# Kernel tuning notes

Measured on AMD Instinct MI355X. Metric: run time of the kernel, lower is better.

The kernel has to match this reference:

```python
import jax, jax.numpy as jnp
import numpy as np

B, T, NC, WD, UNITS = 128, 256, 128, 512, 512
IN_DIM = NC + WD + NC  # x_char + x_word + one-hot prev word


def setup_inputs() -> dict:
    key = jax.random.key(0)
    ks = jax.random.split(key, 7)
    scale = 0.05  # keep gates out of saturation
    return {
        "x_char": jax.random.normal(ks[0], (B, T, NC), jnp.float32),
        "x_word": jax.random.normal(ks[1], (B, T, WD), jnp.float32),
        "W": jax.random.normal(ks[2], (IN_DIM, 4 * UNITS), jnp.float32) * scale,
        "U": jax.random.normal(ks[3], (UNITS, 4 * UNITS), jnp.float32) * scale,
        "b": jnp.zeros((4 * UNITS,), jnp.float32),
        "Ws": jax.random.normal(ks[4], (UNITS, NC), jnp.float32) * scale,
        "bs": jnp.zeros((NC,), jnp.float32),
    }


def reference(x_char, x_word, W, U, b, Ws, bs):
    Bsz, Tlen, nclasses = x_char.shape
    units = U.shape[0]
    # time-major, concat char+word features (matches x_shuffled in original)
    x_t = jnp.concatenate(
        [jnp.swapaxes(x_char, 0, 1), jnp.swapaxes(x_word, 0, 1)], axis=-1
    )  # [T, B, NC+WD]
    word0 = jnp.full((Bsz, nclasses), 1e-5, x_char.dtype)  # start_char
    h0 = jnp.zeros((Bsz, units), x_char.dtype)
    c0 = jnp.zeros((Bsz, units), x_char.dtype)

    def step(carry, x_i):
        word_vec, h, c = carry
        ins = jnp.concatenate([x_i, word_vec], axis=1)  # [B, IN_DIM]
        z = ins @ W + h @ U + b  # [B, 4*units]; Keras gate order i,f,c,o
        zi, zf, zg, zo = jnp.split(z, 4, axis=1)
        i = jax.nn.sigmoid(zi)
        f = jax.nn.sigmoid(zf)
        g = jnp.tanh(zg)
        o = jax.nn.sigmoid(zo)
        c_new = f * c + i * g
        h_new = o * jnp.tanh(c_new)
        probs = jax.nn.softmax(h_new @ Ws + bs, axis=-1)
        idx = jnp.argmax(probs, axis=1)  # [B]
        word_vec_new = jax.nn.one_hot(idx, nclasses, dtype=x_char.dtype)
        return (word_vec_new, h_new, c_new), idx

    _, idxs = jax.lax.scan(step, (word0, h0, c0), x_t)  # idxs: [T, B]
    return jnp.swapaxes(idxs, 0, 1)  # [B, T] int word indices
```

## Files before the change

### kernel.cpp

```cpp
#include <hip/hip_runtime.h>
#include <math.h>

#define BSZ   128
#define TLEN  256
#define NCLS  128
#define WDIM  512
#define XDIM  640
#define G4    2048

#define BT    16
#define JTS   16
#define NBLK  256
#define NTHR  512
#define KCH   8

#define H_OFF     0
#define LPART_OFF 131072
#define W0_OFF    1179648
#define FLAG_OFF  1181696

typedef unsigned long long ull;

__device__ __forceinline__ float sigmoidf_(float x) {
  return 1.0f / (1.0f + expf(-x));
}

__device__ __forceinline__ float4 ld_dev16(const float* p) {
  const ull* q = (const ull*)p;
  ull a = __hip_atomic_load(q,     __ATOMIC_RELAXED, __HIP_MEMORY_SCOPE_AGENT);
  ull b = __hip_atomic_load(q + 1, __ATOMIC_RELAXED, __HIP_MEMORY_SCOPE_AGENT);
  float4 r;
  ((ull*)&r)[0] = a;
  ((ull*)&r)[1] = b;
  return r;
}

__device__ __forceinline__ void st_dev16(float* p, float4 v) {
  ull* q = (ull*)p;
  __hip_atomic_store(q,     ((ull*)&v)[0], __ATOMIC_RELAXED, __HIP_MEMORY_SCOPE_AGENT);
  __hip_atomic_store(q + 1, ((ull*)&v)[1], __ATOMIC_RELAXED, __HIP_MEMORY_SCOPE_AGENT);
}

__global__ void setup_kernel(const float* __restrict__ W,
                             const float* __restrict__ bias,
                             float* __restrict__ ws) {
  int tid = blockIdx.x * blockDim.x + threadIdx.x;
  if (tid < 4096)
    ((unsigned int*)(ws + FLAG_OFF))[tid] = 0u;
  if (tid < G4) {
    float s = 0.0f;
    #pragma unroll 4
    for (int r = 0; r < NCLS; ++r)
      s += W[(size_t)(XDIM + r) * G4 + tid];
    ws[W0_OFF + tid] = bias[tid] + 1e-5f * s;
  }
}

__global__ void __launch_bounds__(NTHR, 1)
lstm_main(const float* __restrict__ xc, const float* __restrict__ xw,
          const float* __restrict__ W,  const float* __restrict__ U,
          const float* __restrict__ bias, const float* __restrict__ Wsm,
          const float* __restrict__ bsv, int* __restrict__ out,
          float* __restrict__ ws)
{
  __shared__ float U_lds[512 * 64];
  __shared__ float ins_lds[2][2176];
  __shared__ float wsm_lds[16 * 128];
  __shared__ float hl_lds[16 * 17];
  __shared__ int   idx_lds[BT];

  float* zred  = &ins_lds[0][0];
  float* Wt    = &ins_lds[0][0];
  float* red_v = zred;
  int*   red_i = (int*)(zred + 528);

  const int tid = threadIdx.x;
  const int blk = blockIdx.x;
  const int grp = blk & 7;
  const int jt  = blk >> 3;
  const int b0  = grp * BT;
  const int j0  = jt * JTS;

  const int gb  = tid & 15;
  const int gg  = (tid >> 4) & 3;
  const int j4  = (tid >> 6) & 3;
  const int kh  = tid >> 8;
  const int c0  = gg * 512 + j0 + j4 * 4;
  const int cc0 = gg * 16 + j4 * 4;

  const int srow = tid >> 5;
  const int sseg = tid & 31;

  const int ub = tid >> 5;
  const int um = tid & 31;

  const int vb = (tid >> 4) & 15;
  const int vj = tid & 15;

  float* hbuf   = ws + H_OFF;
  float* lpart  = ws + LPART_OFF;
  unsigned int* flags = (unsigned int*)(ws + FLAG_OFF);
  unsigned int* myflag   = flags + (grp * 32 + jt) * 16;
  unsigned int* pollflag = flags + (grp * 32 + (tid & 31)) * 16;

  {
    int cc  = tid & 63;
    int col = (cc >> 4) * 512 + j0 + (cc & 15);
    int k0  = tid >> 6;
    for (int kk = 0; kk < 64; ++kk) {
      int k = kk * 8 + k0;
      U_lds[k * 64 + cc] = U[(size_t)k * G4 + col];
    }
  }
  {
    int row = tid >> 5, col4 = tid & 31;
    *(float4*)(&wsm_lds[row * 128 + col4 * 4]) =
        *(const float4*)(Wsm + (size_t)(j0 + row) * NCLS + col4 * 4);
  }

  float4 xq[KCH];
  auto chunk_gemm = [&](int tt0) {
    #pragma unroll
    for (int s = 0; s < KCH; ++s) xq[s] = make_float4(0.f, 0.f, 0.f, 0.f);
    #pragma unroll 1
    for (int kt = 0; kt < 10; ++kt) {
      int id0 = tid,       k0t = id0 >> 4, cg0 = id0 & 15;
      int id1 = tid + 512, k1t = id1 >> 4, cg1 = id1 & 15;
      int col0 = (cg0 >> 2) * 512 + j0 + (cg0 & 3) * 4;
      int col1 = (cg1 >> 2) * 512 + j0 + (cg1 & 3) * 4;
      float4 wv0 = *(const float4*)(W + (size_t)(kt * 64 + k0t) * G4 + col0);
      float4 wv1 = *(const float4*)(W + (size_t)(kt * 64 + k1t) * G4 + col1);
      __syncthreads();
      *(float4*)(Wt + k0t * 64 + cg0 * 4) = wv0;
      *(float4*)(Wt + k1t * 64 + cg1 * 4) = wv1;
      __syncthreads();
      const float* wp = Wt + (kh * 32) * 64 + cc0;
      const float* xb0 = (kt < 2)
        ? xc + ((size_t)(b0 + gb) * TLEN + tt0) * NCLS + kt * 64 + kh * 32
        : xw + ((size_t)(b0 + gb) * TLEN + tt0) * WDIM + (kt * 64 - 128) + kh * 32;
      const size_t xstr = (kt < 2) ? (size_t)NCLS : (size_t)WDIM;
      #pragma unroll
      for (int sb = 0; sb < 2; ++sb) {
        #pragma unroll 1
        for (int q = 0; q < 8; ++q) {
          const float* wq = wp + q * 4 * 64;
          float4 w0 = *(const float4*)(wq);
          float4 w1 = *(const float4*)(wq + 64);
          float4 w2 = *(const float4*)(wq + 128);
          float4 w3 = *(const float4*)(wq + 192);
          const float* xquad = xb0 + (size_t)(sb * 4) * xstr + q * 4;
          #pragma unroll
          for (int u = 0; u < 4; ++u) {
            const int s = sb * 4 + u;
            float4 xa = *(const float4*)(xquad + (size_t)u * xstr);
            xq[s].x = fmaf(xa.x, w0.x, xq[s].x);
            xq[s].y = fmaf(xa.x, w0.y, xq[s].y);
            xq[s].z = fmaf(xa.x, w0.z, xq[s].z);
            xq[s].w = fmaf(xa.x, w0.w, xq[s].w);
            xq[s].x = fmaf(xa.y, w1.x, xq[s].x);
            xq[s].y = fmaf(xa.y, w1.y, xq[s].y);
            xq[s].z = fmaf(xa.y, w1.z, xq[s].z);
            xq[s].w = fmaf(xa.y, w1.w, xq[s].w);
            xq[s].x = fmaf(xa.z, w2.x, xq[s].x);
            xq[s].y = fmaf(xa.z, w2.y, xq[s].y);
            xq[s].z = fmaf(xa.z, w2.z, xq[s].z);
            xq[s].w = fmaf(xa.z, w2.w, xq[s].w);
            xq[s].x = fmaf(xa.w, w3.x, xq[s].x);
            xq[s].y = fmaf(xa.w, w3.y, xq[s].y);
            xq[s].z = fmaf(xa.w, w3.z, xq[s].z);
            xq[s].w = fmaf(xa.w, w3.w, xq[s].w);
          }
          __builtin_amdgcn_sched_barrier(0);
        }
      }
    }
  };

  float creg = 0.0f;

  __syncthreads();
  chunk_gemm(0);
  __syncthreads();

  for (int t = 0; t < TLEN; ++t) {
    float4 acc = xq[0];
    #pragma unroll
    for (int s = 0; s < KCH - 1; ++s) xq[s] = xq[s + 1];

    if (t == 0) {
      if (kh == 0) {
        const float4 w0 = *(const float4*)(ws + W0_OFF + c0);
        acc.x += w0.x; acc.y += w0.y; acc.z += w0.z; acc.w += w0.w;
      }
    } else {
      {
        const float* pb = lpart
            + (((size_t)((t - 1) & 1) * NBLK) + grp * 32) * (BT * NCLS)
            + (size_t)ub * NCLS + um * 4;
        float4 s0 = make_float4(0.f, 0.f, 0.f, 0.f);
        float4 s1 = s0, s2 = s0, s3 = s0;
        #pragma unroll 1
        for (int j2 = 0; j2 < 32; j2 += 4) {
          float4 a = ld_dev16(pb + (size_t)(j2 + 0) * (BT * NCLS));
          float4 b = ld_dev16(pb + (size_t)(j2 + 1) * (BT * NCLS));
          float4 c = ld_dev16(pb + (size_t)(j2 + 2) * (BT * NCLS));
          float4 d = ld_dev16(pb + (size_t)(j2 + 3) * (BT * NCLS));
          s0.x += a.x; s0.y += a.y; s0.z += a.z; s0.w += a.w;
          s1.x += b.x; s1.y += b.y; s1.z += b.z; s1.w += b.w;
          s2.x += c.x; s2.y += c.y; s2.z += c.z; s2.w += c.w;
          s3.x += d.x; s3.y += d.y; s3.z += d.z; s3.w += d.w;
        }
        float4 lv;
        lv.x = (s0.x + s1.x) + (s2.x + s3.x);
        lv.y = (s0.y + s1.y) + (s2.y + s3.y);
        lv.z = (s0.z + s1.z) + (s2.z + s3.z);
        lv.w = (s0.w + s1.w) + (s2.w + s3.w);
        const float4 bb = *(const float4*)(bsv + um * 4);
        float bv = lv.x + bb.x; int bi = um * 4;
        if (lv.y + bb.y > bv) { bv = lv.y + bb.y; bi = um * 4 + 1; }
        if (lv.z + bb.z > bv) { bv = lv.z + bb.z; bi = um * 4 + 2; }
        if (lv.w + bb.w > bv) { bv = lv.w + bb.w; bi = um * 4 + 3; }
        red_v[ub * 33 + um] = bv; red_i[ub * 33 + um] = bi;
        __syncthreads();
        if (um == 0) {
          float v = red_v[ub * 33]; int vi = red_i[ub * 33];
          #pragma unroll
          for (int s = 1; s < 32; ++s) {
            float v2 = red_v[ub * 33 + s];
            int   i2 = red_i[ub * 33 + s];
            if (v2 > v || (v2 == v && i2 < vi)) { v = v2; vi = i2; }
          }
          idx_lds[ub] = vi;
          if (jt == 0) out[(b0 + ub) * TLEN + (t - 1)] = vi;
        }
        __syncthreads();
      }
      if (kh == 0) {
        int wr = XDIM + idx_lds[gb];
        const float4 b4 = *(const float4*)(bias + c0);
        const float4 w4 = *(const float4*)(W + (size_t)wr * G4 + c0);
        acc.x += b4.x + w4.x;  acc.y += b4.y + w4.y;
        acc.z += b4.z + w4.z;  acc.w += b4.w + w4.w;
      }
      {
        const float* hprev = hbuf + ((t + 1) & 1) * (BSZ * 512);
        {
          float4 r = ld_dev16(hprev + (size_t)(b0 + srow) * 512 + sseg * 4);
          *(float4*)(&ins_lds[0][srow * 132 + sseg * 4]) = r;
          __syncthreads();
        }
        #pragma unroll 1
        for (int ch = 0; ch < 4; ++ch) {
          float4 nxt;
          if (ch + 1 < 4) {
            nxt = ld_dev16(hprev + (size_t)(b0 + srow) * 512
                           + (ch + 1) * 128 + sseg * 4);
          }
          const float* up = U_lds + (ch * 128 + kh * 64) * 64 + cc0;
          const float* ip = &ins_lds[ch & 1][gb * 132 + kh * 64];
          #pragma unroll 8
          for (int kk = 0; kk < 64; ++kk) {
            float a = ip[kk];
            float4 u4 = *(const float4*)(up + kk * 64);
            acc.x = fmaf(a, u4.x, acc.x);
            acc.y = fmaf(a, u4.y, acc.y);
            acc.z = fmaf(a, u4.z, acc.z);
            acc.w = fmaf(a, u4.w, acc.w);
          }
          if (ch + 1 < 4) {
            *(float4*)(&ins_lds[(ch + 1) & 1][srow * 132 + sseg * 4]) = nxt;
            __syncthreads();
          }
        }
      }
    }

    *(float4*)(zred + (gb * 2 + kh) * 68 + cc0) = acc;
    __syncthreads();

    if (tid < 256) {
      float zi = zred[(vb * 2) * 68 +  0 + vj] + zred[(vb * 2 + 1) * 68 +  0 + vj];
      float zf = zred[(vb * 2) * 68 + 16 + vj] + zred[(vb * 2 + 1) * 68 + 16 + vj];
      float zg = zred[(vb * 2) * 68 + 32 + vj] + zred[(vb * 2 + 1) * 68 + 32 + vj];
      float zo = zred[(vb * 2) * 68 + 48 + vj] + zred[(vb * 2 + 1) * 68 + 48 + vj];
      float iv = sigmoidf_(zi);
      float fv = sigmoidf_(zf);
      float gv = tanhf(zg);
      float ov = sigmoidf_(zo);
      creg = fv * creg + iv * gv;
      float hn = ov * tanhf(creg);
      __hip_atomic_store(hbuf + (t & 1) * (BSZ * 512)
                         + (size_t)(b0 + vb) * 512 + j0 + vj, hn,
                         __ATOMIC_RELAXED, __HIP_MEMORY_SCOPE_AGENT);
      hl_lds[vb * 17 + vj] = hn;
    }
    __syncthreads();

    {
      float p0 = 0.f, p1 = 0.f, p2 = 0.f, p3 = 0.f;
      #pragma unroll
      for (int j = 0; j < 16; ++j) {
        float hv = hl_lds[ub * 17 + j];
        const float4 wv = *(const float4*)(&wsm_lds[j * 128 + um * 4]);
        p0 = fmaf(hv, wv.x, p0); p1 = fmaf(hv, wv.y, p1);
        p2 = fmaf(hv, wv.z, p2); p3 = fmaf(hv, wv.w, p3);
      }
      float* dst = lpart
          + (((size_t)(t & 1) * NBLK) + (grp * 32 + jt)) * (BT * NCLS)
          + (size_t)ub * NCLS + um * 4;
      st_dev16(dst, make_float4(p0, p1, p2, p3));
    }

    __syncthreads();
    if (tid == 0)
      __hip_atomic_store(myflag, (unsigned)(t + 1),
                         __ATOMIC_RELAXED, __HIP_MEMORY_SCOPE_AGENT);
    if (((t + 1) & (KCH - 1)) == 0 && t + 1 < TLEN)
      chunk_gemm(t + 1);
    if (tid < 64) {
      const unsigned tgt = (unsigned)(t + 1);
      for (;;) {
        unsigned v = __hip_atomic_load(pollflag, __ATOMIC_RELAXED,
                                       __HIP_MEMORY_SCOPE_AGENT);
        if (__all(v >= tgt)) break;
        __builtin_amdgcn_s_sleep(1);
      }
    }
    __syncthreads();
  }

  if (jt == 0) {
    const float* pb = lpart
        + (((size_t)((TLEN - 1) & 1) * NBLK) + grp * 32) * (BT * NCLS)
        + (size_t)ub * NCLS + um * 4;
    float4 s0 = make_float4(0.f, 0.f, 0.f, 0.f);
    float4 s1 = s0, s2 = s0, s3 = s0;
    #pragma unroll 1
    for (int j2 = 0; j2 < 32; j2 += 4) {
      float4 a = ld_dev16(pb + (size_t)(j2 + 0) * (BT * NCLS));
      float4 b = ld_dev16(pb + (size_t)(j2 + 1) * (BT * NCLS));
      float4 c = ld_dev16(pb + (size_t)(j2 + 2) * (BT * NCLS));
      float4 d = ld_dev16(pb + (size_t)(j2 + 3) * (BT * NCLS));
      s0.x += a.x; s0.y += a.y; s0.z += a.z; s0.w += a.w;
      s1.x += b.x; s1.y += b.y; s1.z += b.z; s1.w += b.w;
      s2.x += c.x; s2.y += c.y; s2.z += c.z; s2.w += c.w;
      s3.x += d.x; s3.y += d.y; s3.z += d.z; s3.w += d.w;
    }
    float4 lv;
    lv.x = (s0.x + s1.x) + (s2.x + s3.x);
    lv.y = (s0.y + s1.y) + (s2.y + s3.y);
    lv.z = (s0.z + s1.z) + (s2.z + s3.z);
    lv.w = (s0.w + s1.w) + (s2.w + s3.w);
    const float4 bb = *(const float4*)(bsv + um * 4);
    float bv = lv.x + bb.x; int bi = um * 4;
    if (lv.y + bb.y > bv) { bv = lv.y + bb.y; bi = um * 4 + 1; }
    if (lv.z + bb.z > bv) { bv = lv.z + bb.z; bi = um * 4 + 2; }
    if (lv.w + bb.w > bv) { bv = lv.w + bb.w; bi = um * 4 + 3; }
    __syncthreads();
    red_v[ub * 33 + um] = bv; red_i[ub * 33 + um] = bi;
    __syncthreads();
    if (um == 0) {
      float v = red_v[ub * 33]; int vi = red_i[ub * 33];
      #pragma unroll
      for (int s = 1; s < 32; ++s) {
        float v2 = red_v[ub * 33 + s];
        int   i2 = red_i[ub * 33 + s];
        if (v2 > v || (v2 == v && i2 < vi)) { v = v2; vi = i2; }
      }
      out[(b0 + ub) * TLEN + (TLEN - 1)] = vi;
    }
  }
}

extern "C" void kernel_launch(void* const* d_in, const int* in_sizes, int n_in,
                              void* d_out, int out_size, void* d_ws, size_t ws_size,
                              hipStream_t stream) {
  (void)in_sizes; (void)n_in; (void)out_size; (void)ws_size;
  const float* xc  = (const float*)d_in[0];
  const float* xw  = (const float*)d_in[1];
  const float* W   = (const float*)d_in[2];
  const float* U   = (const float*)d_in[3];
  const float* b   = (const float*)d_in[4];
  const float* Wsm = (const float*)d_in[5];
  const float* bs  = (const float*)d_in[6];
  int*   out = (int*)d_out;
  float* ws  = (float*)d_ws;

  hipLaunchKernelGGL(setup_kernel, dim3(64), dim3(256), 0, stream, W, b, ws);

  void* args[] = { (void*)&xc, (void*)&xw, (void*)&W, (void*)&U, (void*)&b,
                   (void*)&Wsm, (void*)&bs, (void*)&out, (void*)&ws };
  hipLaunchCooperativeKernel((const void*)lstm_main, dim3(NBLK), dim3(NTHR),
                             args, 0, stream);
}
```

Baseline: 9.126 ms.

## Overlap logit partial-sum loads with recurrent h@U GEMM and use shuffle argmax

The global loads that sum the per-block logit partials (for the previous step's argmax) are now interleaved into the h@U accumulation loop, split into groups of four across each chunk half, with sched barriers. This hides their device-memory latency behind LDS FMA work instead of paying it serially before the GEMM. The argmax reduction across 32 lanes now uses wavefront xor shuffles rather than an LDS round trip with an extra barrier. The reordering relies on the partials and the previous h being ready at the same point, and it raises register pressure from the extra in-flight float4 loads.

```diff
diff --git a/kernel.cpp b/kernel.cpp
--- a/kernel.cpp
+++ b/kernel.cpp
@@ -193,23 +193,70 @@
         acc.x += w0.x; acc.y += w0.y; acc.z += w0.z; acc.w += w0.w;
       }
     } else {
+      const float* pb = lpart
+          + (((size_t)((t - 1) & 1) * NBLK) + grp * 32) * (BT * NCLS)
+          + (size_t)ub * NCLS + um * 4;
+      float4 s0 = make_float4(0.f, 0.f, 0.f, 0.f);
+      float4 s1 = s0, s2 = s0, s3 = s0;
+      const float* hprev = hbuf + ((t + 1) & 1) * (BSZ * 512);
       {
-        const float* pb = lpart
-            + (((size_t)((t - 1) & 1) * NBLK) + grp * 32) * (BT * NCLS)
-            + (size_t)ub * NCLS + um * 4;
-        float4 s0 = make_float4(0.f, 0.f, 0.f, 0.f);
-        float4 s1 = s0, s2 = s0, s3 = s0;
-        #pragma unroll 1
-        for (int j2 = 0; j2 < 32; j2 += 4) {
-          float4 a = ld_dev16(pb + (size_t)(j2 + 0) * (BT * NCLS));
-          float4 b = ld_dev16(pb + (size_t)(j2 + 1) * (BT * NCLS));
-          float4 c = ld_dev16(pb + (size_t)(j2 + 2) * (BT * NCLS));
-          float4 d = ld_dev16(pb + (size_t)(j2 + 3) * (BT * NCLS));
-          s0.x += a.x; s0.y += a.y; s0.z += a.z; s0.w += a.w;
-          s1.x += b.x; s1.y += b.y; s1.z += b.z; s1.w += b.w;
-          s2.x += c.x; s2.y += c.y; s2.z += c.z; s2.w += c.w;
-          s3.x += d.x; s3.y += d.y; s3.z += d.z; s3.w += d.w;
-        }
+        float4 r = ld_dev16(hprev + (size_t)(b0 + srow) * 512 + sseg * 4);
+        *(float4*)(&ins_lds[0][srow * 132 + sseg * 4]) = r;
+        __syncthreads();
+      }
+      #pragma unroll 1
+      for (int ch = 0; ch < 4; ++ch) {
+        float4 nxt;
+        if (ch + 1 < 4) {
+          nxt = ld_dev16(hprev + (size_t)(b0 + srow) * 512
+                         + (ch + 1) * 128 + sseg * 4);
+        }
+        const float* up = U_lds + (ch * 128 + kh * 64) * 64 + cc0;
+        const float* ip = &ins_lds[ch & 1][gb * 132 + kh * 64];
+        const float* pbA = pb + (size_t)(8 * ch) * (BT * NCLS);
+        float4 A0 = ld_dev16(pbA + (size_t)0 * (BT * NCLS));
+        float4 A1 = ld_dev16(pbA + (size_t)1 * (BT * NCLS));
+        float4 A2 = ld_dev16(pbA + (size_t)2 * (BT * NCLS));
+        float4 A3 = ld_dev16(pbA + (size_t)3 * (BT * NCLS));
+        #pragma unroll 8
+        for (int kk = 0; kk < 32; ++kk) {
+          float a = ip[kk];
+          float4 u4 = *(const float4*)(up + kk * 64);
+          acc.x = fmaf(a, u4.x, acc.x);
+          acc.y = fmaf(a, u4.y, acc.y);
+          acc.z = fmaf(a, u4.z, acc.z);
+          acc.w = fmaf(a, u4.w, acc.w);
+        }
+        s0.x += A0.x; s0.y += A0.y; s0.z += A0.z; s0.w += A0.w;
+        s1.x += A1.x; s1.y += A1.y; s1.z += A1.z; s1.w += A1.w;
+        s2.x += A2.x; s2.y += A2.y; s2.z += A2.z; s2.w += A2.w;
+        s3.x += A3.x; s3.y += A3.y; s3.z += A3.z; s3.w += A3.w;
+        __builtin_amdgcn_sched_barrier(0);
+        const float* pbB = pb + (size_t)(8 * ch + 4) * (BT * NCLS);
+        float4 B0 = ld_dev16(pbB + (size_t)0 * (BT * NCLS));
+        float4 B1 = ld_dev16(pbB + (size_t)1 * (BT * NCLS));
+        float4 B2 = ld_dev16(pbB + (size_t)2 * (BT * NCLS));
+        float4 B3 = ld_dev16(pbB + (size_t)3 * (BT * NCLS));
+        #pragma unroll 8
+        for (int kk = 32; kk < 64; ++kk) {
+          float a = ip[kk];
+          float4 u4 = *(const float4*)(up + kk * 64);
+          acc.x = fmaf(a, u4.x, acc.x);
+          acc.y = fmaf(a, u4.y, acc.y);
+          acc.z = fmaf(a, u4.z, acc.z);
+          acc.w = fmaf(a, u4.w, acc.w);
+        }
+        s0.x += B0.x; s0.y += B0.y; s0.z += B0.z; s0.w += B0.w;
+        s1.x += B1.x; s1.y += B1.y; s1.z += B1.z; s1.w += B1.w;
+        s2.x += B2.x; s2.y += B2.y; s2.z += B2.z; s2.w += B2.w;
+        s3.x += B3.x; s3.y += B3.y; s3.z += B3.z; s3.w += B3.w;
+        __builtin_amdgcn_sched_barrier(0);
+        if (ch + 1 < 4) {
+          *(float4*)(&ins_lds[(ch + 1) & 1][srow * 132 + sseg * 4]) = nxt;
+          __syncthreads();
+        }
+      }
+      {
         float4 lv;
         lv.x = (s0.x + s1.x) + (s2.x + s3.x);
         lv.y = (s0.y + s1.y) + (s2.y + s3.y);
@@ -220,18 +267,15 @@
         if (lv.y + bb.y > bv) { bv = lv.y + bb.y; bi = um * 4 + 1; }
         if (lv.z + bb.z > bv) { bv = lv.z + bb.z; bi = um * 4 + 2; }
         if (lv.w + bb.w > bv) { bv = lv.w + bb.w; bi = um * 4 + 3; }
-        red_v[ub * 33 + um] = bv; red_i[ub * 33 + um] = bi;
-        __syncthreads();
+        #pragma unroll
+        for (int m = 1; m < 32; m <<= 1) {
+          float ov = __shfl_xor(bv, m, 64);
+          int   oi = __shfl_xor(bi, m, 64);
+          if (ov > bv || (ov == bv && oi < bi)) { bv = ov; bi = oi; }
+        }
         if (um == 0) {
-          float v = red_v[ub * 33]; int vi = red_i[ub * 33];
-          #pragma unroll
-          for (int s = 1; s < 32; ++s) {
-            float v2 = red_v[ub * 33 + s];
-            int   i2 = red_i[ub * 33 + s];
-            if (v2 > v || (v2 == v && i2 < vi)) { v = v2; vi = i2; }
-          }
-          idx_lds[ub] = vi;
-          if (jt == 0) out[(b0 + ub) * TLEN + (t - 1)] = vi;
+          idx_lds[ub] = bi;
+          if (jt == 0) out[(b0 + ub) * TLEN + (t - 1)] = bi;
         }
         __syncthreads();
       }
@@ -241,37 +285,6 @@
         const float4 w4 = *(const float4*)(W + (size_t)wr * G4 + c0);
         acc.x += b4.x + w4.x;  acc.y += b4.y + w4.y;
         acc.z += b4.z + w4.z;  acc.w += b4.w + w4.w;
-      }
-      {
-        const float* hprev = hbuf + ((t + 1) & 1) * (BSZ * 512);
-        {
-          float4 r = ld_dev16(hprev + (size_t)(b0 + srow) * 512 + sseg * 4);
-          *(float4*)(&ins_lds[0][srow * 132 + sseg * 4]) = r;
-          __syncthreads();
-        }
-        #pragma unroll 1
-        for (int ch = 0; ch < 4; ++ch) {
-          float4 nxt;
-          if (ch + 1 < 4) {
-            nxt = ld_dev16(hprev + (size_t)(b0 + srow) * 512
-                           + (ch + 1) * 128 + sseg * 4);
-          }
-          const float* up = U_lds + (ch * 128 + kh * 64) * 64 + cc0;
-          const float* ip = &ins_lds[ch & 1][gb * 132 + kh * 64];
-          #pragma unroll 8
-          for (int kk = 0; kk < 64; ++kk) {
-            float a = ip[kk];
-            float4 u4 = *(const float4*)(up + kk * 64);
-            acc.x = fmaf(a, u4.x, acc.x);
-            acc.y = fmaf(a, u4.y, acc.y);
-            acc.z = fmaf(a, u4.z, acc.z);
-            acc.w = fmaf(a, u4.w, acc.w);
-          }
-          if (ch + 1 < 4) {
-            *(float4*)(&ins_lds[(ch + 1) & 1][srow * 132 + sseg * 4]) = nxt;
-            __syncthreads();
-          }
-        }
       }
     }
 
@@ -356,19 +369,14 @@
     if (lv.y + bb.y > bv) { bv = lv.y + bb.y; bi = um * 4 + 1; }
     if (lv.z + bb.z > bv) { bv = lv.z + bb.z; bi = um * 4 + 2; }
     if (lv.w + bb.w > bv) { bv = lv.w + bb.w; bi = um * 4 + 3; }
-    __syncthreads();
-    red_v[ub * 33 + um] = bv; red_i[ub * 33 + um] = bi;
-    __syncthreads();
-    if (um == 0) {
-      float v = red_v[ub * 33]; int vi = red_i[ub * 33];
-      #pragma unroll
-      for (int s = 1; s < 32; ++s) {
-        float v2 = red_v[ub * 33 + s];
-        int   i2 = red_i[ub * 33 + s];
-        if (v2 > v || (v2 == v && i2 < vi)) { v = v2; vi = i2; }
-      }
-      out[(b0 + ub) * TLEN + (TLEN - 1)] = vi;
-    }
+    #pragma unroll
+    for (int m = 1; m < 32; m <<= 1) {
+      float ov = __shfl_xor(bv, m, 64);
+      int   oi = __shfl_xor(bi, m, 64);
+      if (ov > bv || (ov == bv && oi < bi)) { bv = ov; bi = oi; }
+    }
+    if (um == 0)
+      out[(b0 + ub) * TLEN + (TLEN - 1)] = bi;
   }
 }
 
```

Result: faster. 7.722 ms (-15.4%).
